# Performance work log

Hardware: AMD Instinct MI355X
Metric: run time of the kernel (lower is better)

Reference implementation:

```python
import jax, jax.numpy as jnp
import numpy as np

N = 100000      # nodes
E = 3200000     # edges
NG = 64         # graphs in batch
F_IN, H1, H2 = 128, 128, 64
DENSE = 16 * 8  # first_dense_neurons * second_dense_neurons
LABELS = 2


def setup_inputs() -> dict:
    key = jax.random.key(0)
    ks = jax.random.split(key, 12)
    x = jax.random.normal(ks[0], (N, F_IN), dtype=jnp.float32)
    edge_index = jax.random.randint(ks[1], (2, E), 0, N, dtype=jnp.int32)
    batch = jnp.sort(jax.random.randint(ks[2], (N,), 0, NG, dtype=jnp.int32))
    s = 0.05
    W1 = jax.random.normal(ks[3], (F_IN, H1), dtype=jnp.float32) * s
    b1 = jnp.zeros((H1,), dtype=jnp.float32)
    W2 = jax.random.normal(ks[4], (H1, H2), dtype=jnp.float32) * s
    b2 = jnp.zeros((H2,), dtype=jnp.float32)
    Wf1 = jax.random.normal(ks[5], (H2, DENSE), dtype=jnp.float32) * s
    bf1 = jnp.zeros((DENSE,), dtype=jnp.float32)
    Wf2 = jax.random.normal(ks[6], (DENSE, LABELS), dtype=jnp.float32) * s
    bf2 = jnp.zeros((LABELS,), dtype=jnp.float32)
    return {"x": x, "W1": W1, "b1": b1, "W2": W2, "b2": b2,
            "Wf1": Wf1, "bf1": bf1, "Wf2": Wf2, "bf2": bf2,
            "edge_index": edge_index, "batch": batch}


def _gcn_conv(x, W, b, src, dst, dis):
    # PyG GCNConv: h = x @ W, propagate with sym norm (self-loops included)
    h = x @ W
    coef = (dis[src] * dis[dst])[:, None]          # [E,1]
    agg = jax.ops.segment_sum(h[src] * coef, dst, num_segments=N)
    agg = agg + h * (dis * dis)[:, None]           # self-loop term
    return agg + b


def reference(x, W1, b1, W2, b2, Wf1, bf1, Wf2, bf2, edge_index, batch):
    src, dst = edge_index[0], edge_index[1]
    # degree with self-loops, symmetric normalization D^-1/2 (A+I) D^-1/2
    deg = 1.0 + jax.ops.segment_sum(jnp.ones((E,), x.dtype), dst, num_segments=N)
    dis = jax.lax.rsqrt(deg)
    h1 = jax.nn.relu(_gcn_conv(x, W1, b1, src, dst, dis))
    h2 = jax.nn.relu(_gcn_conv(h1, W2, b2, src, dst, dis))
    a1 = h2 @ Wf1 + bf1                            # [N, DENSE] (dropout: eval mode)
    counts = jax.ops.segment_sum(jnp.ones((N,), x.dtype), batch, num_segments=NG)
    graph_embedding = jax.ops.segment_sum(a1, batch, num_segments=NG) / jnp.maximum(counts, 1.0)[:, None]
    ic_predictions = graph_embedding @ Wf2 + bf2   # [NG, LABELS]
    penalty = jnp.float32(0.0)
    return (graph_embedding, penalty, ic_predictions)
```

## Files before the change

### kernel.cpp

```cpp
#include <hip/hip_runtime.h>


typedef __attribute__((ext_vector_type(8))) short bfrag;
typedef __attribute__((ext_vector_type(16))) float f32x16;
typedef __attribute__((ext_vector_type(2))) float floatx2;

__device__ __forceinline__ unsigned short f2bf(float f) {
    unsigned int u = __builtin_bit_cast(unsigned int, f);
    u = (u + 0x7FFFu + ((u >> 16) & 1u)) >> 16;
    return (unsigned short)u;
}
__device__ __forceinline__ float bf2f(unsigned int lo16) {
    unsigned int v = lo16 << 16;
    return __builtin_bit_cast(float, v);
}
__device__ __forceinline__ unsigned char f2fp8(float f) {
    return (unsigned char)(__builtin_amdgcn_cvt_pk_fp8_f32(f, f, 0, false) & 0xFF);
}
__device__ __forceinline__ void macc8f8(float* acc, const uint2& v, float c) {
    floatx2 f0 = __builtin_amdgcn_cvt_pk_f32_fp8((int)v.x, false);
    floatx2 f1 = __builtin_amdgcn_cvt_pk_f32_fp8((int)v.x, true);
    floatx2 f2 = __builtin_amdgcn_cvt_pk_f32_fp8((int)v.y, false);
    floatx2 f3 = __builtin_amdgcn_cvt_pk_f32_fp8((int)v.y, true);
    acc[0] += f0.x * c; acc[1] += f0.y * c;
    acc[2] += f1.x * c; acc[3] += f1.y * c;
    acc[4] += f2.x * c; acc[5] += f2.y * c;
    acc[6] += f3.x * c; acc[7] += f3.y * c;
}

__global__ __launch_bounds__(256) void bucket_hist_kernel(const int* __restrict__ dst,
                                                          int* __restrict__ bcount, int E) {
    __shared__ int h[256];
    int t = threadIdx.x;
    h[t] = 0;
    __syncthreads();
    int base = blockIdx.x * 4096;
#pragma unroll
    for (int i = 0; i < 16; ++i) {
        int e = base + t + i * 256;
        if (e < E) atomicAdd(&h[dst[e] >> 9], 1);
    }
    __syncthreads();
    if (h[t] > 0) atomicAdd(&bcount[t], h[t]);
}

__global__ void bucket_scan_kernel(const int* __restrict__ bcount, int* __restrict__ bstart,
                                   int* __restrict__ rowstart, int NB, int N, int E) {
    __shared__ int s[256];
    int t = threadIdx.x;
    int v = (t < NB) ? bcount[t] : 0;
    s[t] = v;
    __syncthreads();
    for (int off = 1; off < 256; off <<= 1) {
        int tmp = 0;
        if (t >= off) tmp = s[t - off];
        __syncthreads();
        s[t] += tmp;
        __syncthreads();
    }
    bstart[t] = s[t] - v;
    if (t == 255) bstart[256] = s[255];
    if (t == 0) rowstart[N] = E;
}

__global__ __launch_bounds__(256) void bucket_scatter_kernel(const int* __restrict__ src,
                                                             const int* __restrict__ dst,
                                                             const int* __restrict__ bstart,
                                                             int* __restrict__ bfill,
                                                             unsigned int* __restrict__ stage,
                                                             int E) {
    __shared__ int hist[256];
    __shared__ int abase[256];
    int t = threadIdx.x;
    hist[t] = 0;
    __syncthreads();
    int base = blockIdx.x * 4096;
#pragma unroll
    for (int i = 0; i < 16; ++i) {
        int e = base + t + i * 256;
        if (e < E) atomicAdd(&hist[dst[e] >> 9], 1);
    }
    __syncthreads();
    if (hist[t] > 0) {
        int r = atomicAdd(&bfill[t], hist[t]);
        abase[t] = bstart[t] + r;
    }
    __syncthreads();
    hist[t] = 0;
    __syncthreads();
#pragma unroll
    for (int i = 0; i < 16; ++i) {
        int e = base + t + i * 256;
        if (e < E) {
            int d = dst[e];
            int b = d >> 9;
            int slot = atomicAdd(&hist[b], 1);
            stage[abase[b] + slot] = (unsigned)src[e] | ((unsigned)(d & 511) << 17);
        }
    }
}

__global__ __launch_bounds__(256) void csr_build_kernel(const unsigned int* __restrict__ stage,
                                                        const int* __restrict__ bstart,
                                                        int* __restrict__ rowstart,
                                                        float* __restrict__ dis,
                                                        int* __restrict__ csr_src, int N) {
    __shared__ int cnt[512];
    __shared__ int ofs[512];
    __shared__ int psum[256];
    int b = blockIdx.x, t = threadIdx.x;
    int node0 = b << 9;
    int nb = min(512, N - node0);
    cnt[t] = 0;
    cnt[t + 256] = 0;
    __syncthreads();
    int eb = bstart[b], ee = bstart[b + 1];
    for (int e = eb + t; e < ee; e += 256) {
        unsigned w = stage[e];
        atomicAdd(&cnt[w >> 17], 1);
    }
    __syncthreads();
    int a = cnt[2 * t], c = cnt[2 * t + 1];
    int ps = a + c;
    psum[t] = ps;
    __syncthreads();
    for (int off = 1; off < 256; off <<= 1) {
        int tmp = 0;
        if (t >= off) tmp = psum[t - off];
        __syncthreads();
        psum[t] += tmp;
        __syncthreads();
    }
    int ex = psum[t] - ps;
    ofs[2 * t] = ex;
    ofs[2 * t + 1] = ex + a;
    if (2 * t < nb) {
        rowstart[node0 + 2 * t] = eb + ex;
        dis[node0 + 2 * t] = rsqrtf(1.f + (float)a);
    }
    if (2 * t + 1 < nb) {
        rowstart[node0 + 2 * t + 1] = eb + ex + a;
        dis[node0 + 2 * t + 1] = rsqrtf(1.f + (float)c);
    }
    __syncthreads();
    for (int e = eb + t; e < ee; e += 256) {
        unsigned w = stage[e];
        int l = w >> 17;
        int slot = atomicAdd(&ofs[l], 1);
        csr_src[eb + slot] = (int)(w & 0x1FFFFu);
    }
}

template <int K, int NC>
__global__ __launch_bounds__(256) void wprep_kernel(const float* __restrict__ W,
                                                    unsigned short* __restrict__ Wf) {
    constexpr int CT = NC / 32, KT = K / 16;
    int idx = blockIdx.x * blockDim.x + threadIdx.x;
    if (idx >= KT * CT * 64) return;
    int l = idx & 63;
    int fi = idx >> 6;
    int ct = fi % CT, kt = fi / CT;
    int n = ct * 32 + (l & 31);
    int k0 = kt * 16 + 8 * (l >> 5);
    unsigned short v[8];
#pragma unroll
    for (int j = 0; j < 8; ++j) v[j] = f2bf(W[(size_t)(k0 + j) * NC + n]);
    uint4 o;
    o.x = (unsigned)v[0] | ((unsigned)v[1] << 16);
    o.y = (unsigned)v[2] | ((unsigned)v[3] << 16);
    o.z = (unsigned)v[4] | ((unsigned)v[5] << 16);
    o.w = (unsigned)v[6] | ((unsigned)v[7] << 16);
    *(uint4*)&Wf[(size_t)idx * 8] = o;
}

template <int K, int NC, bool IN_F32>
__global__ __launch_bounds__(256) void gemm_mfma_kernel(const void* __restrict__ Av,
                                                        const unsigned short* __restrict__ Wf,
                                                        unsigned char* __restrict__ C,
                                                        int M) {
    constexpr int KT = K / 16, CT = NC / 32;
    int wid = (blockIdx.x * blockDim.x + threadIdx.x) >> 6;
    int lane = threadIdx.x & 63;
    int row0 = wid * 32;
    if (row0 >= M) return;

    bfrag B[KT][CT];
#pragma unroll
    for (int kt = 0; kt < KT; ++kt)
#pragma unroll
        for (int ct = 0; ct < CT; ++ct)
            B[kt][ct] = *(const bfrag*)&Wf[(size_t)((kt * CT + ct) * 64 + lane) * 8];

    f32x16 acc[CT];
#pragma unroll
    for (int ct = 0; ct < CT; ++ct)
#pragma unroll
        for (int i = 0; i < 16; ++i) acc[ct][i] = 0.f;

    int r = row0 + (lane & 31);
    if (r >= M) r = M - 1;
#pragma unroll
    for (int kt = 0; kt < KT; ++kt) {
        bfrag a;
        if (IN_F32) {
            const float* Arow = &((const float*)Av)[(size_t)r * K + 8 * (lane >> 5)];
            float4 v0 = *(const float4*)&Arow[kt * 16];
            float4 v1 = *(const float4*)&Arow[kt * 16 + 4];
            a[0] = (short)f2bf(v0.x); a[1] = (short)f2bf(v0.y);
            a[2] = (short)f2bf(v0.z); a[3] = (short)f2bf(v0.w);
            a[4] = (short)f2bf(v1.x); a[5] = (short)f2bf(v1.y);
            a[6] = (short)f2bf(v1.z); a[7] = (short)f2bf(v1.w);
        } else {
            const unsigned short* Arow =
                &((const unsigned short*)Av)[(size_t)r * K + 8 * (lane >> 5)];
            a = *(const bfrag*)&Arow[kt * 16];
        }
#pragma unroll
        for (int ct = 0; ct < CT; ++ct)
            acc[ct] = __builtin_amdgcn_mfma_f32_32x32x16_bf16(a, B[kt][ct], acc[ct], 0, 0, 0);
    }

    int colb = lane & 31;
    int rowq = 4 * (lane >> 5);
#pragma unroll
    for (int ct = 0; ct < CT; ++ct) {
        int col = ct * 32 + colb;
#pragma unroll
        for (int rg = 0; rg < 16; ++rg) {
            int row = row0 + (rg & 3) + 8 * (rg >> 2) + rowq;
            if (row < M) C[(size_t)row * NC + col] = f2fp8(acc[ct][rg]);
        }
    }
}

template <int NC>
__global__ __launch_bounds__(256) void aggregate_kernel(const unsigned char* __restrict__ h,
                                                        const float* __restrict__ dis,
                                                        const int* __restrict__ rowstart,
                                                        const int* __restrict__ csr_src,
                                                        const float* __restrict__ bias,
                                                        unsigned short* __restrict__ out,
                                                        int N) {
    constexpr int LPR = NC / 8;
    constexpr int RPS = 64 / LPR;
    int wid = (blockIdx.x * blockDim.x + threadIdx.x) >> 6;
    int lane = threadIdx.x & 63;
    if (wid >= N) return;
    int n = wid;
    int sub = lane / LPR;
    int fid = lane % LPR;
    const uint2* h8 = (const uint2*)h;
    float d = dis[n];
    float acc[8];
#pragma unroll
    for (int i = 0; i < 8; ++i) acc[i] = 0.f;
    if (sub == 0) {
        uint2 hv = h8[(size_t)n * LPR + fid];
        macc8f8(acc, hv, d);
    }

    int beg = rowstart[n], end = rowstart[n + 1];
    for (int e0 = beg; e0 < end; e0 += 64) {
        int idx = e0 + lane;
        int sv = 0;
        float dv = 0.f;
        if (idx < end) { sv = csr_src[idx]; dv = dis[sv]; }
        int cnt = min(64, end - e0);
        int j = 0;
        for (; j + 2 * RPS <= cnt; j += 2 * RPS) {
            int ja = j + sub, jb = j + RPS + sub;
            int sa = __shfl(sv, ja); float ca = __shfl(dv, ja);
            int sb = __shfl(sv, jb); float cb = __shfl(dv, jb);
            uint2 va = h8[(size_t)sa * LPR + fid];
            uint2 vb = h8[(size_t)sb * LPR + fid];
            macc8f8(acc, va, ca);
            macc8f8(acc, vb, cb);
        }
        for (; j < cnt; j += RPS) {
            int jj = j + sub;
            int jc = min(jj, cnt - 1);
            int s = __shfl(sv, jc);
            float c = __shfl(dv, jc);
            if (jj >= cnt) c = 0.f;
            uint2 v = h8[(size_t)s * LPR + fid];
            macc8f8(acc, v, c);
        }
    }
#pragma unroll
    for (int m = LPR; m < 64; m <<= 1) {
#pragma unroll
        for (int i = 0; i < 8; ++i) acc[i] += __shfl_xor(acc[i], m);
    }
    if (sub == 0) {
        const float4 bv0 = *(const float4*)&bias[fid * 8 + 0];
        const float4 bv1 = *(const float4*)&bias[fid * 8 + 4];
        float r[8];
        r[0] = fmaxf(acc[0] * d + bv0.x, 0.f);
        r[1] = fmaxf(acc[1] * d + bv0.y, 0.f);
        r[2] = fmaxf(acc[2] * d + bv0.z, 0.f);
        r[3] = fmaxf(acc[3] * d + bv0.w, 0.f);
        r[4] = fmaxf(acc[4] * d + bv1.x, 0.f);
        r[5] = fmaxf(acc[5] * d + bv1.y, 0.f);
        r[6] = fmaxf(acc[6] * d + bv1.z, 0.f);
        r[7] = fmaxf(acc[7] * d + bv1.w, 0.f);
        uint4 o;
        o.x = (unsigned)f2bf(r[0]) | ((unsigned)f2bf(r[1]) << 16);
        o.y = (unsigned)f2bf(r[2]) | ((unsigned)f2bf(r[3]) << 16);
        o.z = (unsigned)f2bf(r[4]) | ((unsigned)f2bf(r[5]) << 16);
        o.w = (unsigned)f2bf(r[6]) | ((unsigned)f2bf(r[7]) << 16);
        *(uint4*)&out[(size_t)n * NC + fid * 8] = o;
    }
}

__global__ __launch_bounds__(64) void pool_kernel(const unsigned short* __restrict__ h2,
                                                  const int* __restrict__ batch,
                                                  float* __restrict__ gsum, int N) {
    int f = threadIdx.x;
    int n0 = blockIdx.x * 128;
    int nend = min(n0 + 128, N);
    float acc = 0.f;
    int gcur = batch[n0];
    for (int n = n0; n < nend; ++n) {
        int g = batch[n];
        if (g != gcur) {
            atomicAdd(&gsum[gcur * 64 + f], acc);
            acc = 0.f;
            gcur = g;
        }
        acc += bf2f(h2[(size_t)n * 64 + f]);
    }
    atomicAdd(&gsum[gcur * 64 + f], acc);
}

__global__ __launch_bounds__(256) void count_batch_kernel(const int* __restrict__ batch,
                                                          int* __restrict__ gcnt, int N) {
    __shared__ int lc[64];
    int t = threadIdx.x;
    if (t < 64) lc[t] = 0;
    __syncthreads();
    int n = blockIdx.x * blockDim.x + t;
    if (n < N) atomicAdd(&lc[batch[n]], 1);
    __syncthreads();
    if (t < 64 && lc[t] > 0) atomicAdd(&gcnt[t], lc[t]);
}

__global__ __launch_bounds__(128) void head_kernel(const float* __restrict__ gsum,
                                                   const int* __restrict__ gcnt,
                                                   const float* __restrict__ Wf1,
                                                   const float* __restrict__ bf1,
                                                   const float* __restrict__ Wf2,
                                                   const float* __restrict__ bf2,
                                                   float* __restrict__ out) {
    __shared__ float ph[64];
    __shared__ float red0[128], red1[128];
    int g = blockIdx.x, f = threadIdx.x;
    if (f < 64) ph[f] = gsum[g * 64 + f] / (float)max(gcnt[g], 1);
    __syncthreads();
    float ge = bf1[f];
#pragma unroll 8
    for (int k = 0; k < 64; ++k) ge += ph[k] * Wf1[k * 128 + f];
    out[g * 128 + f] = ge;
    red0[f] = ge * Wf2[f * 2 + 0];
    red1[f] = ge * Wf2[f * 2 + 1];
    __syncthreads();
    for (int off = 64; off > 0; off >>= 1) {
        if (f < off) { red0[f] += red0[f + off]; red1[f] += red1[f + off]; }
        __syncthreads();
    }
    if (f == 0) {
        out[8192 + 1 + g * 2 + 0] = red0[0] + bf2[0];
        out[8192 + 1 + g * 2 + 1] = red1[0] + bf2[1];
        if (g == 0) out[8192] = 0.f;
    }
}

extern "C" void kernel_launch(void* const* d_in, const int* in_sizes, int n_in,
                              void* d_out, int out_size, void* d_ws, size_t ws_size,
                              hipStream_t stream) {
    const float* x   = (const float*)d_in[0];
    const float* W1  = (const float*)d_in[1];
    const float* b1  = (const float*)d_in[2];
    const float* W2  = (const float*)d_in[3];
    const float* b2  = (const float*)d_in[4];
    const float* Wf1 = (const float*)d_in[5];
    const float* bf1 = (const float*)d_in[6];
    const float* Wf2 = (const float*)d_in[7];
    const float* bf2 = (const float*)d_in[8];
    const int* edge  = (const int*)d_in[9];
    const int* batch = (const int*)d_in[10];

    const int N = in_sizes[10];
    const int E = in_sizes[9] / 2;
    const int* srcA = edge;
    const int* dstA = edge + E;
    float* out = (float*)d_out;

    const int NB = (N + 511) >> 9;

    char* p = (char*)d_ws;
    auto alloc = [&](size_t bytes) {
        char* r = p;
        p += (bytes + 255) & ~(size_t)255;
        return r;
    };
    float* gsum     = (float*)alloc(64 * 64 * 4);
    int*   gcnt     = (int*)alloc(64 * 4);
    int*   bcount   = (int*)alloc(256 * 4);
    int*   bfill    = (int*)alloc(256 * 4);
    size_t zbytes   = (size_t)(p - (char*)d_ws);
    int*   bstart   = (int*)alloc(260 * 4);
    float* dis      = (float*)alloc((size_t)N * 4);
    int*   rowstart = (int*)alloc((size_t)(N + 1) * 4);
    unsigned short* Wp1 = (unsigned short*)alloc(8 * 4 * 64 * 8 * 2);
    unsigned short* Wp2 = (unsigned short*)alloc(8 * 2 * 64 * 8 * 2);
    unsigned int* stage = (unsigned int*)alloc((size_t)E * 4);
    int*   csr_src  = (int*)alloc((size_t)E * 4);
    unsigned char*  hf8   = (unsigned char*)alloc((size_t)N * 128);
    unsigned short* h1b   = (unsigned short*)alloc((size_t)N * 128 * 2);
    unsigned short* h2b   = (unsigned short*)alloc((size_t)N * 64 * 2);

    hipMemsetAsync(d_ws, 0, zbytes, stream);

    const int EB = (E + 4095) / 4096;
    bucket_hist_kernel<<<EB, 256, 0, stream>>>(dstA, bcount, E);
    bucket_scan_kernel<<<1, 256, 0, stream>>>(bcount, bstart, rowstart, NB, N, E);
    bucket_scatter_kernel<<<EB, 256, 0, stream>>>(srcA, dstA, bstart, bfill, stage, E);
    csr_build_kernel<<<NB, 256, 0, stream>>>(stage, bstart, rowstart, dis, csr_src, N);

    wprep_kernel<128, 128><<<8, 256, 0, stream>>>(W1, Wp1);
    wprep_kernel<128, 64><<<4, 256, 0, stream>>>(W2, Wp2);

    const int GB = (N + 127) / 128;
    gemm_mfma_kernel<128, 128, true><<<GB, 256, 0, stream>>>(x, Wp1, hf8, N);
    aggregate_kernel<128><<<(N + 3) / 4, 256, 0, stream>>>(hf8, dis, rowstart, csr_src,
                                                           b1, h1b, N);
    gemm_mfma_kernel<128, 64, false><<<GB, 256, 0, stream>>>(h1b, Wp2, hf8, N);
    aggregate_kernel<64><<<(N + 3) / 4, 256, 0, stream>>>(hf8, dis, rowstart, csr_src,
                                                          b2, h2b, N);
    pool_kernel<<<(N + 127) / 128, 64, 0, stream>>>(h2b, batch, gsum, N);
    count_batch_kernel<<<(N + 255) / 256, 256, 0, stream>>>(batch, gcnt, N);
    head_kernel<<<64, 128, 0, stream>>>(gsum, gcnt, Wf1, bf1, Wf2, bf2, out);
}
```

Baseline: 426.3 us.

## Widen aggregate gathers to 16 bytes, privatize histograms, stream GEMM weights

```diff
diff --git a/kernel.cpp b/kernel.cpp
--- a/kernel.cpp
+++ b/kernel.cpp
@@ -17,31 +17,35 @@
 __device__ __forceinline__ unsigned char f2fp8(float f) {
     return (unsigned char)(__builtin_amdgcn_cvt_pk_fp8_f32(f, f, 0, false) & 0xFF);
 }
-__device__ __forceinline__ void macc8f8(float* acc, const uint2& v, float c) {
-    floatx2 f0 = __builtin_amdgcn_cvt_pk_f32_fp8((int)v.x, false);
-    floatx2 f1 = __builtin_amdgcn_cvt_pk_f32_fp8((int)v.x, true);
-    floatx2 f2 = __builtin_amdgcn_cvt_pk_f32_fp8((int)v.y, false);
-    floatx2 f3 = __builtin_amdgcn_cvt_pk_f32_fp8((int)v.y, true);
-    acc[0] += f0.x * c; acc[1] += f0.y * c;
-    acc[2] += f1.x * c; acc[3] += f1.y * c;
-    acc[4] += f2.x * c; acc[5] += f2.y * c;
-    acc[6] += f3.x * c; acc[7] += f3.y * c;
+__device__ __forceinline__ void macc16f8(float* acc, const uint4& v, float c) {
+    floatx2 f;
+    f = __builtin_amdgcn_cvt_pk_f32_fp8((int)v.x, false); acc[0] += f.x * c;  acc[1] += f.y * c;
+    f = __builtin_amdgcn_cvt_pk_f32_fp8((int)v.x, true);  acc[2] += f.x * c;  acc[3] += f.y * c;
+    f = __builtin_amdgcn_cvt_pk_f32_fp8((int)v.y, false); acc[4] += f.x * c;  acc[5] += f.y * c;
+    f = __builtin_amdgcn_cvt_pk_f32_fp8((int)v.y, true);  acc[6] += f.x * c;  acc[7] += f.y * c;
+    f = __builtin_amdgcn_cvt_pk_f32_fp8((int)v.z, false); acc[8] += f.x * c;  acc[9] += f.y * c;
+    f = __builtin_amdgcn_cvt_pk_f32_fp8((int)v.z, true);  acc[10] += f.x * c; acc[11] += f.y * c;
+    f = __builtin_amdgcn_cvt_pk_f32_fp8((int)v.w, false); acc[12] += f.x * c; acc[13] += f.y * c;
+    f = __builtin_amdgcn_cvt_pk_f32_fp8((int)v.w, true);  acc[14] += f.x * c; acc[15] += f.y * c;
 }
 
 __global__ __launch_bounds__(256) void bucket_hist_kernel(const int* __restrict__ dst,
                                                           int* __restrict__ bcount, int E) {
-    __shared__ int h[256];
+    __shared__ int h[4][256];
     int t = threadIdx.x;
-    h[t] = 0;
+    int c = t & 3;
+#pragma unroll
+    for (int q = 0; q < 4; ++q) h[q][t] = 0;
     __syncthreads();
     int base = blockIdx.x * 4096;
 #pragma unroll
     for (int i = 0; i < 16; ++i) {
         int e = base + t + i * 256;
-        if (e < E) atomicAdd(&h[dst[e] >> 9], 1);
-    }
-    __syncthreads();
-    if (h[t] > 0) atomicAdd(&bcount[t], h[t]);
+        if (e < E) atomicAdd(&h[c][dst[e] >> 9], 1);
+    }
+    __syncthreads();
+    int s = h[0][t] + h[1][t] + h[2][t] + h[3][t];
+    if (s > 0) atomicAdd(&bcount[t], s);
 }
 
 __global__ void bucket_scan_kernel(const int* __restrict__ bcount, int* __restrict__ bstart,
@@ -69,24 +73,33 @@
                                                              int* __restrict__ bfill,
                                                              unsigned int* __restrict__ stage,
                                                              int E) {
-    __shared__ int hist[256];
-    __shared__ int abase[256];
+    __shared__ int hist[4][256];
+    __shared__ int cbase[4][256];
     int t = threadIdx.x;
-    hist[t] = 0;
+    int c = t & 3;
+#pragma unroll
+    for (int q = 0; q < 4; ++q) hist[q][t] = 0;
     __syncthreads();
     int base = blockIdx.x * 4096;
 #pragma unroll
     for (int i = 0; i < 16; ++i) {
         int e = base + t + i * 256;
-        if (e < E) atomicAdd(&hist[dst[e] >> 9], 1);
-    }
-    __syncthreads();
-    if (hist[t] > 0) {
-        int r = atomicAdd(&bfill[t], hist[t]);
-        abase[t] = bstart[t] + r;
-    }
-    __syncthreads();
-    hist[t] = 0;
+        if (e < E) atomicAdd(&hist[c][dst[e] >> 9], 1);
+    }
+    __syncthreads();
+    int h0 = hist[0][t], h1 = hist[1][t], h2 = hist[2][t], h3 = hist[3][t];
+    int tot = h0 + h1 + h2 + h3;
+    if (tot > 0) {
+        int r = atomicAdd(&bfill[t], tot);
+        int b0 = bstart[t] + r;
+        cbase[0][t] = b0;
+        cbase[1][t] = b0 + h0;
+        cbase[2][t] = b0 + h0 + h1;
+        cbase[3][t] = b0 + h0 + h1 + h2;
+    }
+    __syncthreads();
+#pragma unroll
+    for (int q = 0; q < 4; ++q) hist[q][t] = 0;
     __syncthreads();
 #pragma unroll
     for (int i = 0; i < 16; ++i) {
@@ -94,8 +107,8 @@
         if (e < E) {
             int d = dst[e];
             int b = d >> 9;
-            int slot = atomicAdd(&hist[b], 1);
-            stage[abase[b] + slot] = (unsigned)src[e] | ((unsigned)(d & 511) << 17);
+            int slot = atomicAdd(&hist[c][b], 1);
+            stage[cbase[c][b] + slot] = (unsigned)src[e] | ((unsigned)(d & 511) << 17);
         }
     }
 }
@@ -184,13 +197,6 @@
     int row0 = wid * 32;
     if (row0 >= M) return;
 
-    bfrag B[KT][CT];
-#pragma unroll
-    for (int kt = 0; kt < KT; ++kt)
-#pragma unroll
-        for (int ct = 0; ct < CT; ++ct)
-            B[kt][ct] = *(const bfrag*)&Wf[(size_t)((kt * CT + ct) * 64 + lane) * 8];
-
     f32x16 acc[CT];
 #pragma unroll
     for (int ct = 0; ct < CT; ++ct)
@@ -199,7 +205,7 @@
 
     int r = row0 + (lane & 31);
     if (r >= M) r = M - 1;
-#pragma unroll
+#pragma unroll 1
     for (int kt = 0; kt < KT; ++kt) {
         bfrag a;
         if (IN_F32) {
@@ -216,8 +222,10 @@
             a = *(const bfrag*)&Arow[kt * 16];
         }
 #pragma unroll
-        for (int ct = 0; ct < CT; ++ct)
-            acc[ct] = __builtin_amdgcn_mfma_f32_32x32x16_bf16(a, B[kt][ct], acc[ct], 0, 0, 0);
+        for (int ct = 0; ct < CT; ++ct) {
+            bfrag b = *(const bfrag*)&Wf[(size_t)((kt * CT + ct) * 64 + lane) * 8];
+            acc[ct] = __builtin_amdgcn_mfma_f32_32x32x16_bf16(a, b, acc[ct], 0, 0, 0);
+        }
     }
 
     int colb = lane & 31;
@@ -241,7 +249,7 @@
                                                         const float* __restrict__ bias,
                                                         unsigned short* __restrict__ out,
                                                         int N) {
-    constexpr int LPR = NC / 8;
+    constexpr int LPR = NC / 16;
     constexpr int RPS = 64 / LPR;
     int wid = (blockIdx.x * blockDim.x + threadIdx.x) >> 6;
     int lane = threadIdx.x & 63;
@@ -249,14 +257,14 @@
     int n = wid;
     int sub = lane / LPR;
     int fid = lane % LPR;
-    const uint2* h8 = (const uint2*)h;
+    const uint4* h16 = (const uint4*)h;
     float d = dis[n];
-    float acc[8];
-#pragma unroll
-    for (int i = 0; i < 8; ++i) acc[i] = 0.f;
+    float acc[16];
+#pragma unroll
+    for (int i = 0; i < 16; ++i) acc[i] = 0.f;
     if (sub == 0) {
-        uint2 hv = h8[(size_t)n * LPR + fid];
-        macc8f8(acc, hv, d);
+        uint4 hv = h16[(size_t)n * LPR + fid];
+        macc16f8(acc, hv, d);
     }
 
     int beg = rowstart[n], end = rowstart[n + 1];
@@ -271,10 +279,10 @@
             int ja = j + sub, jb = j + RPS + sub;
             int sa = __shfl(sv, ja); float ca = __shfl(dv, ja);
             int sb = __shfl(sv, jb); float cb = __shfl(dv, jb);
-            uint2 va = h8[(size_t)sa * LPR + fid];
-            uint2 vb = h8[(size_t)sb * LPR + fid];
-            macc8f8(acc, va, ca);
-            macc8f8(acc, vb, cb);
+            uint4 va = h16[(size_t)sa * LPR + fid];
+            uint4 vb = h16[(size_t)sb * LPR + fid];
+            macc16f8(acc, va, ca);
+            macc16f8(acc, vb, cb);
         }
         for (; j < cnt; j += RPS) {
             int jj = j + sub;
@@ -282,33 +290,36 @@
             int s = __shfl(sv, jc);
             float c = __shfl(dv, jc);
             if (jj >= cnt) c = 0.f;
-            uint2 v = h8[(size_t)s * LPR + fid];
-            macc8f8(acc, v, c);
+            uint4 v = h16[(size_t)s * LPR + fid];
+            macc16f8(acc, v, c);
         }
     }
 #pragma unroll
     for (int m = LPR; m < 64; m <<= 1) {
 #pragma unroll
-        for (int i = 0; i < 8; ++i) acc[i] += __shfl_xor(acc[i], m);
+        for (int i = 0; i < 16; ++i) acc[i] += __shfl_xor(acc[i], m);
     }
     if (sub == 0) {
-        const float4 bv0 = *(const float4*)&bias[fid * 8 + 0];
-        const float4 bv1 = *(const float4*)&bias[fid * 8 + 4];
-        float r[8];
-        r[0] = fmaxf(acc[0] * d + bv0.x, 0.f);
-        r[1] = fmaxf(acc[1] * d + bv0.y, 0.f);
-        r[2] = fmaxf(acc[2] * d + bv0.z, 0.f);
-        r[3] = fmaxf(acc[3] * d + bv0.w, 0.f);
-        r[4] = fmaxf(acc[4] * d + bv1.x, 0.f);
-        r[5] = fmaxf(acc[5] * d + bv1.y, 0.f);
-        r[6] = fmaxf(acc[6] * d + bv1.z, 0.f);
-        r[7] = fmaxf(acc[7] * d + bv1.w, 0.f);
-        uint4 o;
-        o.x = (unsigned)f2bf(r[0]) | ((unsigned)f2bf(r[1]) << 16);
-        o.y = (unsigned)f2bf(r[2]) | ((unsigned)f2bf(r[3]) << 16);
-        o.z = (unsigned)f2bf(r[4]) | ((unsigned)f2bf(r[5]) << 16);
-        o.w = (unsigned)f2bf(r[6]) | ((unsigned)f2bf(r[7]) << 16);
-        *(uint4*)&out[(size_t)n * NC + fid * 8] = o;
+        float r[16];
+#pragma unroll
+        for (int q = 0; q < 4; ++q) {
+            float4 bv = *(const float4*)&bias[fid * 16 + q * 4];
+            r[q * 4 + 0] = fmaxf(acc[q * 4 + 0] * d + bv.x, 0.f);
+            r[q * 4 + 1] = fmaxf(acc[q * 4 + 1] * d + bv.y, 0.f);
+            r[q * 4 + 2] = fmaxf(acc[q * 4 + 2] * d + bv.z, 0.f);
+            r[q * 4 + 3] = fmaxf(acc[q * 4 + 3] * d + bv.w, 0.f);
+        }
+        uint4 o0, o1;
+        o0.x = (unsigned)f2bf(r[0]) | ((unsigned)f2bf(r[1]) << 16);
+        o0.y = (unsigned)f2bf(r[2]) | ((unsigned)f2bf(r[3]) << 16);
+        o0.z = (unsigned)f2bf(r[4]) | ((unsigned)f2bf(r[5]) << 16);
+        o0.w = (unsigned)f2bf(r[6]) | ((unsigned)f2bf(r[7]) << 16);
+        o1.x = (unsigned)f2bf(r[8]) | ((unsigned)f2bf(r[9]) << 16);
+        o1.y = (unsigned)f2bf(r[10]) | ((unsigned)f2bf(r[11]) << 16);
+        o1.z = (unsigned)f2bf(r[12]) | ((unsigned)f2bf(r[13]) << 16);
+        o1.w = (unsigned)f2bf(r[14]) | ((unsigned)f2bf(r[15]) << 16);
+        *(uint4*)&out[(size_t)n * NC + fid * 16] = o0;
+        *(uint4*)&out[(size_t)n * NC + fid * 16 + 8] = o1;
     }
 }
 
```

After: 464.2 us. 8.9% more time.

## Replicate LDS histograms, pack fp8 accumulate into float2, fuse node counting into pool

Applied to the files above, without the earlier changes.

```diff
diff --git a/kernel.cpp b/kernel.cpp
--- a/kernel.cpp
+++ b/kernel.cpp
@@ -17,31 +17,30 @@
 __device__ __forceinline__ unsigned char f2fp8(float f) {
     return (unsigned char)(__builtin_amdgcn_cvt_pk_fp8_f32(f, f, 0, false) & 0xFF);
 }
-__device__ __forceinline__ void macc8f8(float* acc, const uint2& v, float c) {
-    floatx2 f0 = __builtin_amdgcn_cvt_pk_f32_fp8((int)v.x, false);
-    floatx2 f1 = __builtin_amdgcn_cvt_pk_f32_fp8((int)v.x, true);
-    floatx2 f2 = __builtin_amdgcn_cvt_pk_f32_fp8((int)v.y, false);
-    floatx2 f3 = __builtin_amdgcn_cvt_pk_f32_fp8((int)v.y, true);
-    acc[0] += f0.x * c; acc[1] += f0.y * c;
-    acc[2] += f1.x * c; acc[3] += f1.y * c;
-    acc[4] += f2.x * c; acc[5] += f2.y * c;
-    acc[6] += f3.x * c; acc[7] += f3.y * c;
+__device__ __forceinline__ void macc8f8(floatx2* acc, const uint2& v, floatx2 c2) {
+    acc[0] += __builtin_amdgcn_cvt_pk_f32_fp8((int)v.x, false) * c2;
+    acc[1] += __builtin_amdgcn_cvt_pk_f32_fp8((int)v.x, true) * c2;
+    acc[2] += __builtin_amdgcn_cvt_pk_f32_fp8((int)v.y, false) * c2;
+    acc[3] += __builtin_amdgcn_cvt_pk_f32_fp8((int)v.y, true) * c2;
 }
 
 __global__ __launch_bounds__(256) void bucket_hist_kernel(const int* __restrict__ dst,
                                                           int* __restrict__ bcount, int E) {
-    __shared__ int h[256];
+    __shared__ int h[4][256];
     int t = threadIdx.x;
-    h[t] = 0;
+    int c = t & 3;
+#pragma unroll
+    for (int q = 0; q < 4; ++q) h[q][t] = 0;
     __syncthreads();
     int base = blockIdx.x * 4096;
 #pragma unroll
     for (int i = 0; i < 16; ++i) {
         int e = base + t + i * 256;
-        if (e < E) atomicAdd(&h[dst[e] >> 9], 1);
-    }
-    __syncthreads();
-    if (h[t] > 0) atomicAdd(&bcount[t], h[t]);
+        if (e < E) atomicAdd(&h[c][dst[e] >> 9], 1);
+    }
+    __syncthreads();
+    int s = h[0][t] + h[1][t] + h[2][t] + h[3][t];
+    if (s > 0) atomicAdd(&bcount[t], s);
 }
 
 __global__ void bucket_scan_kernel(const int* __restrict__ bcount, int* __restrict__ bstart,
@@ -69,24 +68,33 @@
                                                              int* __restrict__ bfill,
                                                              unsigned int* __restrict__ stage,
                                                              int E) {
-    __shared__ int hist[256];
-    __shared__ int abase[256];
+    __shared__ int hist[4][256];
+    __shared__ int cbase[4][256];
     int t = threadIdx.x;
-    hist[t] = 0;
+    int c = t & 3;
+#pragma unroll
+    for (int q = 0; q < 4; ++q) hist[q][t] = 0;
     __syncthreads();
     int base = blockIdx.x * 4096;
 #pragma unroll
     for (int i = 0; i < 16; ++i) {
         int e = base + t + i * 256;
-        if (e < E) atomicAdd(&hist[dst[e] >> 9], 1);
-    }
-    __syncthreads();
-    if (hist[t] > 0) {
-        int r = atomicAdd(&bfill[t], hist[t]);
-        abase[t] = bstart[t] + r;
-    }
-    __syncthreads();
-    hist[t] = 0;
+        if (e < E) atomicAdd(&hist[c][dst[e] >> 9], 1);
+    }
+    __syncthreads();
+    int h0 = hist[0][t], h1 = hist[1][t], h2 = hist[2][t], h3 = hist[3][t];
+    int tot = h0 + h1 + h2 + h3;
+    if (tot > 0) {
+        int r = atomicAdd(&bfill[t], tot);
+        int b0 = bstart[t] + r;
+        cbase[0][t] = b0;
+        cbase[1][t] = b0 + h0;
+        cbase[2][t] = b0 + h0 + h1;
+        cbase[3][t] = b0 + h0 + h1 + h2;
+    }
+    __syncthreads();
+#pragma unroll
+    for (int q = 0; q < 4; ++q) hist[q][t] = 0;
     __syncthreads();
 #pragma unroll
     for (int i = 0; i < 16; ++i) {
@@ -94,8 +102,8 @@
         if (e < E) {
             int d = dst[e];
             int b = d >> 9;
-            int slot = atomicAdd(&hist[b], 1);
-            stage[abase[b] + slot] = (unsigned)src[e] | ((unsigned)(d & 511) << 17);
+            int slot = atomicAdd(&hist[c][b], 1);
+            stage[cbase[c][b] + slot] = (unsigned)src[e] | ((unsigned)(d & 511) << 17);
         }
     }
 }
@@ -251,12 +259,13 @@
     int fid = lane % LPR;
     const uint2* h8 = (const uint2*)h;
     float d = dis[n];
-    float acc[8];
-#pragma unroll
-    for (int i = 0; i < 8; ++i) acc[i] = 0.f;
+    floatx2 acc[4];
+#pragma unroll
+    for (int i = 0; i < 4; ++i) acc[i] = (floatx2)(0.f);
     if (sub == 0) {
         uint2 hv = h8[(size_t)n * LPR + fid];
-        macc8f8(acc, hv, d);
+        floatx2 d2 = {d, d};
+        macc8f8(acc, hv, d2);
     }
 
     int beg = rowstart[n], end = rowstart[n + 1];
@@ -273,8 +282,9 @@
             int sb = __shfl(sv, jb); float cb = __shfl(dv, jb);
             uint2 va = h8[(size_t)sa * LPR + fid];
             uint2 vb = h8[(size_t)sb * LPR + fid];
-            macc8f8(acc, va, ca);
-            macc8f8(acc, vb, cb);
+            floatx2 ca2 = {ca, ca}, cb2 = {cb, cb};
+            macc8f8(acc, va, ca2);
+            macc8f8(acc, vb, cb2);
         }
         for (; j < cnt; j += RPS) {
             int jj = j + sub;
@@ -283,26 +293,30 @@
             float c = __shfl(dv, jc);
             if (jj >= cnt) c = 0.f;
             uint2 v = h8[(size_t)s * LPR + fid];
-            macc8f8(acc, v, c);
+            floatx2 c2 = {c, c};
+            macc8f8(acc, v, c2);
         }
     }
 #pragma unroll
     for (int m = LPR; m < 64; m <<= 1) {
 #pragma unroll
-        for (int i = 0; i < 8; ++i) acc[i] += __shfl_xor(acc[i], m);
+        for (int i = 0; i < 4; ++i) {
+            acc[i].x += __shfl_xor(acc[i].x, m);
+            acc[i].y += __shfl_xor(acc[i].y, m);
+        }
     }
     if (sub == 0) {
         const float4 bv0 = *(const float4*)&bias[fid * 8 + 0];
         const float4 bv1 = *(const float4*)&bias[fid * 8 + 4];
         float r[8];
-        r[0] = fmaxf(acc[0] * d + bv0.x, 0.f);
-        r[1] = fmaxf(acc[1] * d + bv0.y, 0.f);
-        r[2] = fmaxf(acc[2] * d + bv0.z, 0.f);
-        r[3] = fmaxf(acc[3] * d + bv0.w, 0.f);
-        r[4] = fmaxf(acc[4] * d + bv1.x, 0.f);
-        r[5] = fmaxf(acc[5] * d + bv1.y, 0.f);
-        r[6] = fmaxf(acc[6] * d + bv1.z, 0.f);
-        r[7] = fmaxf(acc[7] * d + bv1.w, 0.f);
+        r[0] = fmaxf(acc[0].x * d + bv0.x, 0.f);
+        r[1] = fmaxf(acc[0].y * d + bv0.y, 0.f);
+        r[2] = fmaxf(acc[1].x * d + bv0.z, 0.f);
+        r[3] = fmaxf(acc[1].y * d + bv0.w, 0.f);
+        r[4] = fmaxf(acc[2].x * d + bv1.x, 0.f);
+        r[5] = fmaxf(acc[2].y * d + bv1.y, 0.f);
+        r[6] = fmaxf(acc[3].x * d + bv1.z, 0.f);
+        r[7] = fmaxf(acc[3].y * d + bv1.w, 0.f);
         uint4 o;
         o.x = (unsigned)f2bf(r[0]) | ((unsigned)f2bf(r[1]) << 16);
         o.y = (unsigned)f2bf(r[2]) | ((unsigned)f2bf(r[3]) << 16);
@@ -314,34 +328,28 @@
 
 __global__ __launch_bounds__(64) void pool_kernel(const unsigned short* __restrict__ h2,
                                                   const int* __restrict__ batch,
-                                                  float* __restrict__ gsum, int N) {
+                                                  float* __restrict__ gsum,
+                                                  int* __restrict__ gcnt, int N) {
     int f = threadIdx.x;
     int n0 = blockIdx.x * 128;
     int nend = min(n0 + 128, N);
     float acc = 0.f;
+    int run = 0;
     int gcur = batch[n0];
     for (int n = n0; n < nend; ++n) {
         int g = batch[n];
         if (g != gcur) {
             atomicAdd(&gsum[gcur * 64 + f], acc);
+            if (f == 0) atomicAdd(&gcnt[gcur], run);
             acc = 0.f;
+            run = 0;
             gcur = g;
         }
         acc += bf2f(h2[(size_t)n * 64 + f]);
+        run++;
     }
     atomicAdd(&gsum[gcur * 64 + f], acc);
-}
-
-__global__ __launch_bounds__(256) void count_batch_kernel(const int* __restrict__ batch,
-                                                          int* __restrict__ gcnt, int N) {
-    __shared__ int lc[64];
-    int t = threadIdx.x;
-    if (t < 64) lc[t] = 0;
-    __syncthreads();
-    int n = blockIdx.x * blockDim.x + t;
-    if (n < N) atomicAdd(&lc[batch[n]], 1);
-    __syncthreads();
-    if (t < 64 && lc[t] > 0) atomicAdd(&gcnt[t], lc[t]);
+    if (f == 0) atomicAdd(&gcnt[gcur], run);
 }
 
 __global__ __launch_bounds__(128) void head_kernel(const float* __restrict__ gsum,
@@ -437,7 +445,6 @@
     gemm_mfma_kernel<128, 64, false><<<GB, 256, 0, stream>>>(h1b, Wp2, hf8, N);
     aggregate_kernel<64><<<(N + 3) / 4, 256, 0, stream>>>(hf8, dis, rowstart, csr_src,
                                                           b2, h2b, N);
-    pool_kernel<<<(N + 127) / 128, 64, 0, stream>>>(h2b, batch, gsum, N);
-    count_batch_kernel<<<(N + 255) / 256, 256, 0, stream>>>(batch, gcnt, N);
+    pool_kernel<<<(N + 127) / 128, 64, 0, stream>>>(h2b, batch, gsum, gcnt, N);
     head_kernel<<<64, 128, 0, stream>>>(gsum, gcnt, Wf1, bf1, Wf2, bf2, out);
 }
```

New measurement: 433.4 us. Within noise of the previous version (+1.7%).
